# Kernel tuning notes

Hardware: AMD Instinct MI355X
Metric: run time of the kernel (lower is better)

The kernel has to match this reference:

```python
import jax, jax.numpy as jnp
import numpy as np
from jax import lax

B, N, C, RED = 8, 2048, 1024, 4
GN_EPS = 1e-5


def setup_inputs() -> dict:
    key = jax.random.key(0)
    ks = jax.random.split(key, 8)
    s = lambda k, shp, sc: jax.random.normal(k, shp, jnp.float32) * sc
    return dict(
        x=jax.random.normal(ks[0], (B, N, C), jnp.float32),
        qkv_w=s(ks[1], (C, 3 * C), 0.02),
        c1=jnp.float32(0.01 ** 2),
        c2=jnp.float32(0.03 ** 2),
        conv1_w=s(ks[2], (4, 1, 3), 0.3),      # OIH
        gn_g=jnp.ones(4, jnp.float32),
        gn_b=jnp.zeros(4, jnp.float32),
        conv2_w=s(ks[3], (1, 4, 3), 0.3),      # OIH
        conv2_b=jnp.zeros(1, jnp.float32),
        ch_w1=s(ks[4], (C, C // RED), 0.02),
        ch_b1=jnp.zeros(C // RED, jnp.float32),
        ch_w2=s(ks[5], (C // RED, C), 0.02),
        ch_b2=jnp.zeros(C, jnp.float32),
        proj_w=s(ks[6], (C, C), 0.02),
        proj_b=jnp.zeros(C, jnp.float32),
    )


def _conv1d(x, w):  # x:[B,Cin,N], w:[O,I,3], pad=1
    return lax.conv_general_dilated(x, w, (1,), [(1, 1)],
                                    dimension_numbers=('NCH', 'OIH', 'NCH'))


def _ode_func(A, conv1_w, gn_g, gn_b, conv2_w, conv2_b):
    # A: [B,N] -> Conv1d(1,4) -> GroupNorm(2,4) -> ReLU -> Conv1d(4,1)
    h = _conv1d(A[:, None, :], conv1_w)                 # [B,4,N]
    b, _, n = h.shape
    hg = h.reshape(b, 2, 2, n)                          # 2 groups of 2 channels
    mu = hg.mean((2, 3), keepdims=True)
    var = hg.var((2, 3), keepdims=True)
    h = ((hg - mu) * lax.rsqrt(var + GN_EPS)).reshape(b, 4, n)
    h = jax.nn.relu(h * gn_g[None, :, None] + gn_b[None, :, None])
    y = _conv1d(h, conv2_w) + conv2_b[None, :, None]    # [B,1,N]
    return y[:, 0, :]


def reference(x, qkv_w, c1, c2, conv1_w, gn_g, gn_b, conv2_w, conv2_b,
              ch_w1, ch_b1, ch_w2, ch_b2, proj_w, proj_b):
    Bx, Nx, Cx = x.shape
    qkv = (x @ qkv_w).reshape(Bx, Nx, 3, Cx)
    q, k, v = qkv[..., 0, :], qkv[..., 1, :], qkv[..., 2, :]

    # SSIM-style per-token statistics over the channel dim
    mu_q = q.mean(-1, keepdims=True)
    mu_k = k.mean(-1, keepdims=True)
    dq, dk = q - mu_q, k - mu_k
    inv_cm1 = 1.0 / (Cx - 1)
    sigma_qk = (dq * dk).sum(-1, keepdims=True) * inv_cm1
    sigma_q2 = (dq * dq).sum(-1, keepdims=True) * inv_cm1
    sigma_k2 = (dk * dk).sum(-1, keepdims=True) * inv_cm1
    num = (2 * mu_q * mu_k + c1) * (2 * sigma_qk + c2)
    den = (mu_q ** 2 + mu_k ** 2 + c1) * (sigma_q2 + sigma_k2 + c2)
    attn_base = ((num / (den + 1e-7)) ** 2)[..., 0]     # [B,N]

    # explicit-Euler integration over t = linspace(0,1,2) -> one step, dt=1
    steps = 2
    ts = jnp.linspace(0.0, 1.0, steps)
    dts = ts[1:] - ts[:-1]

    def step(A, dt):
        return A + dt * _ode_func(A, conv1_w, gn_g, gn_b, conv2_w, conv2_b), None

    A, _ = lax.scan(step, attn_base, dts)
    final_a = jax.nn.sigmoid(A)                         # [B,N]
    weights = jax.nn.softmax(final_a, axis=1)           # softmax over tokens

    # channel gating from mean token
    m = x.mean(axis=1, keepdims=True)                   # [B,1,C]
    ch_w = jax.nn.sigmoid(jax.nn.relu(m @ ch_w1 + ch_b1) @ ch_w2 + ch_b2)

    out_low = weights[..., None] * v * ch_w             # [B,N,C]
    return out_low @ proj_w + proj_b
```

## Files before the change

kernel.cpp:

```cpp
#include <hip/hip_runtime.h>

typedef __attribute__((ext_vector_type(8))) short short8;
typedef __attribute__((ext_vector_type(4))) short short4v;
typedef __attribute__((ext_vector_type(4))) float floatx4;

__device__ __forceinline__ unsigned short f2bf(float f) {
    unsigned u = __float_as_uint(f);
    u = u + 0x7fffu + ((u >> 16) & 1u);
    return (unsigned short)(u >> 16);
}
__device__ __forceinline__ float bf2f(short s) {
    return __uint_as_float(((unsigned)(unsigned short)s) << 16);
}

__device__ __forceinline__ void gl_lds16(const void* g, void* l) {
    __builtin_amdgcn_global_load_lds((const __attribute__((address_space(1))) void*)g,
                                     (__attribute__((address_space(3))) void*)l, 16, 0, 0);
}

__global__ __launch_bounds__(256) void convmean_kernel(const float* __restrict__ x,
                                                       short* __restrict__ xb,
                                                       float* __restrict__ part) {
    int bid = blockIdx.x;
    int b = bid >> 6, nch = bid & 63;
    int tid = threadIdx.x;
    size_t base = ((size_t)b * 2048 + nch * 32) * 1024;
    float s0 = 0.f, s1 = 0.f, s2 = 0.f, s3 = 0.f;
    int c0 = tid * 4;
    for (int r = 0; r < 32; r++) {
        const float* rp = x + base + (size_t)r * 1024 + c0;
        float4 v = *(const float4*)rp;
        s0 += v.x; s1 += v.y; s2 += v.z; s3 += v.w;
        short4v o;
        o[0] = (short)f2bf(v.x); o[1] = (short)f2bf(v.y);
        o[2] = (short)f2bf(v.z); o[3] = (short)f2bf(v.w);
        *(short4v*)(xb + base + (size_t)r * 1024 + c0) = o;
    }
    float* pp = part + ((size_t)b * 64 + nch) * 1024 + c0;
    float4 ps; ps.x = s0; ps.y = s1; ps.z = s2; ps.w = s3;
    *(float4*)pp = ps;
}

__global__ __launch_bounds__(256) void transpose_conv_kernel(const float* __restrict__ w_qkv,
                                                             short* __restrict__ qkvT,
                                                             const float* __restrict__ w_proj,
                                                             short* __restrict__ projT) {
    __shared__ float t[64][65];
    int bx = blockIdx.x;
    const float* in; short* out; int C;
    int c0, r0 = blockIdx.y * 64;
    if (bx < 48) { in = w_qkv; out = qkvT; C = 3072; c0 = bx * 64; }
    else         { in = w_proj; out = projT; C = 1024; c0 = (bx - 48) * 64; }
    int tid = threadIdx.x;
#pragma unroll
    for (int l = 0; l < 16; l++) {
        int idx = l * 256 + tid;
        int rr = idx >> 6, cc = idx & 63;
        t[rr][cc] = in[(size_t)(r0 + rr) * C + c0 + cc];
    }
    __syncthreads();
#pragma unroll
    for (int l = 0; l < 16; l++) {
        int idx = l * 256 + tid;
        int rr = idx >> 6, cc = idx & 63;
        out[(size_t)(c0 + rr) * 1024 + r0 + cc] = (short)f2bf(t[cc][rr]);
    }
}

__global__ __launch_bounds__(256) void ch_kernel(const float* __restrict__ part,
                                                 const float* __restrict__ w1,
                                                 const float* __restrict__ b1,
                                                 const float* __restrict__ w2,
                                                 const float* __restrict__ b2,
                                                 float* __restrict__ ch) {
    int b = blockIdx.x, tid = threadIdx.x;
    __shared__ float mrow[1024];
    __shared__ float hid[256];
    for (int i = tid; i < 1024; i += 256) {
        float s = 0.f;
        for (int j = 0; j < 64; j++) s += part[((size_t)b * 64 + j) * 1024 + i];
        mrow[i] = s * (1.f / 2048.f);
    }
    __syncthreads();
    {
        float s = 0.f;
        for (int i = 0; i < 1024; i++) s += mrow[i] * w1[(size_t)i * 256 + tid];
        hid[tid] = fmaxf(s + b1[tid], 0.f);
    }
    __syncthreads();
    for (int c = tid; c < 1024; c += 256) {
        float s = 0.f;
        for (int j = 0; j < 256; j++) s += hid[j] * w2[(size_t)j * 1024 + c];
        ch[(size_t)b * 1024 + c] = 1.f / (1.f + expf(-(s + b2[c])));
    }
}

__global__ __launch_bounds__(256) void gemm_qkv_kernel(const short* __restrict__ A,
                                                       const short* __restrict__ BT,
                                                       short* __restrict__ Cout,
                                                       const float* __restrict__ ch)
{
    __shared__ __align__(16) short Ash[2 * 128 * 32];
    __shared__ __align__(16) short Bsh[2 * 128 * 32];
    const int tid = threadIdx.x;
    const int wave = tid >> 6, lane = tid & 63;
    const int id = blockIdx.x;
    const int xcd = id & 7, j = id >> 3;
    const int bm = (j & 15) * 8 + xcd;
    const int bn = j >> 4;
    const int wm = wave >> 1, wn = wave & 1;
    const int l4 = lane >> 2, kk = (lane & 3) * 8;
    const int lda = 1024, ldb = 1024;

    const short* Ag = A + (size_t)(bm * 128 + wave * 32 + l4) * lda + kk;
    const short* Bg = BT + (size_t)(bn * 128 + wave * 32 + l4) * ldb + kk;
    short* lA = Ash + wave * 1024;
    short* lB = Bsh + wave * 1024;

    floatx4 acc[4][4];
    floatx4 zero = {0.f, 0.f, 0.f, 0.f};
#pragma unroll
    for (int i = 0; i < 4; i++)
#pragma unroll
        for (int jj = 0; jj < 4; jj++) acc[i][jj] = zero;

    const int ar = lane & 15, ak = (lane >> 4) * 8;

    for (int k0 = 0; k0 < 1024; k0 += 64) {
#pragma unroll
        for (int h = 0; h < 2; h++) {
            gl_lds16(Ag + k0 + h * 32, lA + h * 4096);
            gl_lds16(Ag + 16 * lda + k0 + h * 32, lA + h * 4096 + 512);
            gl_lds16(Bg + k0 + h * 32, lB + h * 4096);
            gl_lds16(Bg + 16 * ldb + k0 + h * 32, lB + h * 4096 + 512);
        }
        __syncthreads();
#pragma unroll
        for (int h = 0; h < 2; h++) {
            short8 af[4], bfr[4];
#pragma unroll
            for (int t = 0; t < 4; t++)
                af[t] = *(const short8*)(Ash + h * 4096 + (wm * 64 + t * 16 + ar) * 32 + ak);
#pragma unroll
            for (int t = 0; t < 4; t++)
                bfr[t] = *(const short8*)(Bsh + h * 4096 + (wn * 64 + t * 16 + ar) * 32 + ak);
#pragma unroll
            for (int i = 0; i < 4; i++)
#pragma unroll
                for (int jj = 0; jj < 4; jj++)
                    acc[i][jj] = __builtin_amdgcn_mfma_f32_16x16x32_bf16(af[i], bfr[jj], acc[i][jj], 0, 0, 0);
        }
        __syncthreads();
    }

    const int row0 = bm * 128 + wm * 64;
    const int col0 = bn * 128 + wn * 64;
#pragma unroll
    for (int i = 0; i < 4; i++) {
#pragma unroll
        for (int jj = 0; jj < 4; jj++) {
            int col = col0 + jj * 16 + (lane & 15);
#pragma unroll
            for (int r = 0; r < 4; r++) {
                int row = row0 + i * 16 + (lane >> 4) * 4 + r;
                float v = acc[i][jj][r];
                if (col >= 2048) v *= ch[(size_t)((row >> 11) << 10) + (col - 2048)];
                Cout[(size_t)row * 3072 + col] = (short)f2bf(v);
            }
        }
    }
}

__global__ __launch_bounds__(256) void stats_kernel(const short* __restrict__ qkv,
                                                    const float* __restrict__ c1p,
                                                    const float* __restrict__ c2p,
                                                    float* __restrict__ attn) {
    int row = blockIdx.x * 4 + (threadIdx.x >> 6);
    int lane = threadIdx.x & 63;
    const short* q = qkv + (size_t)row * 3072;
    const short* k = q + 1024;
    float sq = 0.f, sk = 0.f, sqq = 0.f, skk = 0.f, sqk = 0.f;
#pragma unroll
    for (int j = 0; j < 2; j++) {
        int idx = j * 512 + lane * 8;
        short8 qv = *(const short8*)(q + idx);
        short8 kv = *(const short8*)(k + idx);
#pragma unroll
        for (int e = 0; e < 8; e++) {
            float qf = bf2f(qv[e]), kf = bf2f(kv[e]);
            sq += qf; sk += kf;
            sqq += qf * qf; skk += kf * kf; sqk += qf * kf;
        }
    }
#pragma unroll
    for (int m = 1; m < 64; m <<= 1) {
        sq += __shfl_xor(sq, m);
        sk += __shfl_xor(sk, m);
        sqq += __shfl_xor(sqq, m);
        skk += __shfl_xor(skk, m);
        sqk += __shfl_xor(sqk, m);
    }
    if (lane == 0) {
        const float C = 1024.f, invcm1 = 1.f / 1023.f;
        float c1 = *c1p, c2 = *c2p;
        float muq = sq / C, muk = sk / C;
        float sigqk = (sqk - C * muq * muk) * invcm1;
        float sigq2 = (sqq - C * muq * muq) * invcm1;
        float sigk2 = (skk - C * muk * muk) * invcm1;
        float num = (2.f * muq * muk + c1) * (2.f * sigqk + c2);
        float den = (muq * muq + muk * muk + c1) * (sigq2 + sigk2 + c2);
        float r = num / (den + 1e-7f);
        attn[row] = r * r;
    }
}

__device__ __forceinline__ float blk_sum(float v, float* buf) {
#pragma unroll
    for (int m = 1; m < 64; m <<= 1) v += __shfl_xor(v, m);
    int wave = threadIdx.x >> 6;
    if ((threadIdx.x & 63) == 0) buf[wave] = v;
    __syncthreads();
    float r = buf[0] + buf[1] + buf[2] + buf[3];
    __syncthreads();
    return r;
}
__device__ __forceinline__ float blk_max(float v, float* buf) {
#pragma unroll
    for (int m = 1; m < 64; m <<= 1) v = fmaxf(v, __shfl_xor(v, m));
    int wave = threadIdx.x >> 6;
    if ((threadIdx.x & 63) == 0) buf[wave] = v;
    __syncthreads();
    float r = fmaxf(fmaxf(buf[0], buf[1]), fmaxf(buf[2], buf[3]));
    __syncthreads();
    return r;
}

__global__ __launch_bounds__(256) void ode_softmax_kernel(const float* __restrict__ attn,
                                                          const float* __restrict__ w1,
                                                          const float* __restrict__ gng,
                                                          const float* __restrict__ gnb,
                                                          const float* __restrict__ w2,
                                                          const float* __restrict__ b2,
                                                          float* __restrict__ wgt) {
    int b = blockIdx.x, tid = threadIdx.x;
    __shared__ float A0[2048];
    __shared__ float H[4][2048];
    __shared__ float rbuf[4];
    for (int i = tid; i < 2048; i += 256) A0[i] = attn[(size_t)b * 2048 + i];
    __syncthreads();
    float w1l[12], w2l[12];
#pragma unroll
    for (int i = 0; i < 12; i++) { w1l[i] = w1[i]; w2l[i] = w2[i]; }
    float gg[4], gb[4];
#pragma unroll
    for (int c = 0; c < 4; c++) { gg[c] = gng[c]; gb[c] = gnb[c]; }

    float s0 = 0.f, ss0 = 0.f, s1 = 0.f, ss1 = 0.f;
    for (int i = tid; i < 2048; i += 256) {
        float le = (i > 0) ? A0[i - 1] : 0.f;
        float mi = A0[i];
        float ri = (i < 2047) ? A0[i + 1] : 0.f;
#pragma unroll
        for (int c = 0; c < 4; c++) {
            float h = w1l[c * 3] * le + w1l[c * 3 + 1] * mi + w1l[c * 3 + 2] * ri;
            H[c][i] = h;
            if (c < 2) { s0 += h; ss0 += h * h; } else { s1 += h; ss1 += h * h; }
        }
    }
    s0 = blk_sum(s0, rbuf);
    ss0 = blk_sum(ss0, rbuf);
    s1 = blk_sum(s1, rbuf);
    ss1 = blk_sum(ss1, rbuf);
    float mu0 = s0 / 4096.f, var0 = ss0 / 4096.f - mu0 * mu0;
    float mu1 = s1 / 4096.f, var1 = ss1 / 4096.f - mu1 * mu1;
    float is0 = 1.f / sqrtf(var0 + 1e-5f);
    float is1 = 1.f / sqrtf(var1 + 1e-5f);

    for (int i = tid; i < 2048; i += 256) {
#pragma unroll
        for (int c = 0; c < 4; c++) {
            float inv = (c < 2) ? is0 : is1;
            float mu = (c < 2) ? mu0 : mu1;
            float v = (H[c][i] - mu) * inv * gg[c] + gb[c];
            H[c][i] = fmaxf(v, 0.f);
        }
    }
    __syncthreads();

    float bias2 = b2[0];
    float myfa[8];
    float lmax = -1e30f;
#pragma unroll
    for (int ii = 0; ii < 8; ii++) {
        int i = tid + ii * 256;
        float y = bias2;
#pragma unroll
        for (int c = 0; c < 4; c++) {
            float le = (i > 0) ? H[c][i - 1] : 0.f;
            float mi = H[c][i];
            float ri = (i < 2047) ? H[c][i + 1] : 0.f;
            y += w2l[c * 3] * le + w2l[c * 3 + 1] * mi + w2l[c * 3 + 2] * ri;
        }
        float Av = A0[i] + y;
        float fa = 1.f / (1.f + expf(-Av));
        myfa[ii] = fa;
        lmax = fmaxf(lmax, fa);
    }
    float gmax = blk_max(lmax, rbuf);
    float lsum = 0.f;
#pragma unroll
    for (int ii = 0; ii < 8; ii++) {
        myfa[ii] = expf(myfa[ii] - gmax);
        lsum += myfa[ii];
    }
    float gsum = blk_sum(lsum, rbuf);
    float inv = 1.f / gsum;
#pragma unroll
    for (int ii = 0; ii < 8; ii++) wgt[(size_t)b * 2048 + tid + ii * 256] = myfa[ii] * inv;
}

__global__ __launch_bounds__(256) void gemm_out_kernel(const short* __restrict__ qkv,
                                                       const short* __restrict__ BT,
                                                       const float* __restrict__ wgt,
                                                       const float* __restrict__ pb,
                                                       float* __restrict__ Out)
{
    __shared__ __align__(16) short Ash[2 * 128 * 32];
    __shared__ __align__(16) short Bsh[2 * 128 * 32];
    const int tid = threadIdx.x;
    const int wave = tid >> 6, lane = tid & 63;
    const int id = blockIdx.x;
    const int xcd = id & 7, j = id >> 3;
    const int bm = (j & 15) * 8 + xcd;
    const int bn = j >> 4;
    const int wm = wave >> 1, wn = wave & 1;
    const int l4 = lane >> 2, kk = (lane & 3) * 8;
    const int lda = 3072, ldb = 1024;
    const short* A = qkv + 2048;

    const short* Ag = A + (size_t)(bm * 128 + wave * 32 + l4) * lda + kk;
    const short* Bg = BT + (size_t)(bn * 128 + wave * 32 + l4) * ldb + kk;
    short* lA = Ash + wave * 1024;
    short* lB = Bsh + wave * 1024;

    floatx4 acc[4][4];
    floatx4 zero = {0.f, 0.f, 0.f, 0.f};
#pragma unroll
    for (int i = 0; i < 4; i++)
#pragma unroll
        for (int jj = 0; jj < 4; jj++) acc[i][jj] = zero;

    const int ar = lane & 15, ak = (lane >> 4) * 8;

    for (int k0 = 0; k0 < 1024; k0 += 64) {
#pragma unroll
        for (int h = 0; h < 2; h++) {
            gl_lds16(Ag + k0 + h * 32, lA + h * 4096);
            gl_lds16(Ag + 16 * lda + k0 + h * 32, lA + h * 4096 + 512);
            gl_lds16(Bg + k0 + h * 32, lB + h * 4096);
            gl_lds16(Bg + 16 * ldb + k0 + h * 32, lB + h * 4096 + 512);
        }
        __syncthreads();
#pragma unroll
        for (int h = 0; h < 2; h++) {
            short8 af[4], bfr[4];
#pragma unroll
            for (int t = 0; t < 4; t++)
                af[t] = *(const short8*)(Ash + h * 4096 + (wm * 64 + t * 16 + ar) * 32 + ak);
#pragma unroll
            for (int t = 0; t < 4; t++)
                bfr[t] = *(const short8*)(Bsh + h * 4096 + (wn * 64 + t * 16 + ar) * 32 + ak);
#pragma unroll
            for (int i = 0; i < 4; i++)
#pragma unroll
                for (int jj = 0; jj < 4; jj++)
                    acc[i][jj] = __builtin_amdgcn_mfma_f32_16x16x32_bf16(af[i], bfr[jj], acc[i][jj], 0, 0, 0);
        }
        __syncthreads();
    }

    const int row0 = bm * 128 + wm * 64;
    const int col0 = bn * 128 + wn * 64;
#pragma unroll
    for (int i = 0; i < 4; i++) {
#pragma unroll
        for (int jj = 0; jj < 4; jj++) {
            int col = col0 + jj * 16 + (lane & 15);
            float bias = pb[col];
#pragma unroll
            for (int r = 0; r < 4; r++) {
                int row = row0 + i * 16 + (lane >> 4) * 4 + r;
                Out[(size_t)row * 1024 + col] = wgt[row] * acc[i][jj][r] + bias;
            }
        }
    }
}

extern "C" void kernel_launch(void* const* d_in, const int* in_sizes, int n_in,
                              void* d_out, int out_size, void* d_ws, size_t ws_size,
                              hipStream_t stream) {
    const float* x       = (const float*)d_in[0];
    const float* qkv_w   = (const float*)d_in[1];
    const float* c1      = (const float*)d_in[2];
    const float* c2      = (const float*)d_in[3];
    const float* conv1_w = (const float*)d_in[4];
    const float* gn_g    = (const float*)d_in[5];
    const float* gn_b    = (const float*)d_in[6];
    const float* conv2_w = (const float*)d_in[7];
    const float* conv2_b = (const float*)d_in[8];
    const float* ch_w1   = (const float*)d_in[9];
    const float* ch_b1   = (const float*)d_in[10];
    const float* ch_w2   = (const float*)d_in[11];
    const float* ch_b2   = (const float*)d_in[12];
    const float* proj_w  = (const float*)d_in[13];
    const float* proj_b  = (const float*)d_in[14];
    float* out = (float*)d_out;

    size_t off = 0;
    char* base = (char*)d_ws;
    auto carve = [&](size_t bytes) -> char* {
        char* p = base + off;
        off += (bytes + 255) & ~(size_t)255;
        return p;
    };
    short* x_bf  = (short*)carve((size_t)16777216 * 2);
    short* qkvT  = (short*)carve((size_t)3072 * 1024 * 2);
    short* projT = (short*)carve((size_t)1024 * 1024 * 2);
    short* qkv   = (short*)carve((size_t)16384 * 3072 * 2);
    float* attn  = (float*)carve((size_t)16384 * 4);
    float* wgt   = (float*)carve((size_t)16384 * 4);
    float* part  = (float*)carve((size_t)8 * 64 * 1024 * 4);
    float* chw   = (float*)carve((size_t)8 * 1024 * 4);

    convmean_kernel<<<512, 256, 0, stream>>>(x, x_bf, part);
    transpose_conv_kernel<<<dim3(64, 16), 256, 0, stream>>>(qkv_w, qkvT, proj_w, projT);
    ch_kernel<<<8, 256, 0, stream>>>(part, ch_w1, ch_b1, ch_w2, ch_b2, chw);
    gemm_qkv_kernel<<<3072, 256, 0, stream>>>(x_bf, qkvT, qkv, chw);
    stats_kernel<<<4096, 256, 0, stream>>>(qkv, c1, c2, attn);
    ode_softmax_kernel<<<8, 256, 0, stream>>>(attn, conv1_w, gn_g, gn_b, conv2_w, conv2_b, wgt);
    gemm_out_kernel<<<1024, 256, 0, stream>>>(qkv, projT, wgt, proj_b, out);
}
```

Baseline: 456.2 us.

## Fuse SSIM q/k statistics into QKV GEMM epilogue and skip writing q,k

Interleaves q and k weight rows so each GEMM tile holds paired q/k columns, and computes per-row partial sums (sum q, sum k, q², k², qk) in the epilogue instead of storing q and k. A small finalize kernel reduces the 16 partials into the SSIM attention value, which removes the stats kernel and the q/k write and read traffic. V is written to a compact buffer through LDS-staged, vectorized stores. The output GEMM also stages its results in LDS for coalesced float4 stores. Block-to-tile mapping is reordered in both GEMMs. Computing statistics from fp32 accumulators rather than bf16-rounded values slightly changes numerics.

```diff
diff --git a/kernel.cpp b/kernel.cpp
--- a/kernel.cpp
+++ b/kernel.cpp
@@ -47,10 +47,10 @@
                                                              short* __restrict__ projT) {
     __shared__ float t[64][65];
     int bx = blockIdx.x;
-    const float* in; short* out; int C;
+    const float* in; short* out; int C; bool is_qkv;
     int c0, r0 = blockIdx.y * 64;
-    if (bx < 48) { in = w_qkv; out = qkvT; C = 3072; c0 = bx * 64; }
-    else         { in = w_proj; out = projT; C = 1024; c0 = (bx - 48) * 64; }
+    if (bx < 48) { in = w_qkv; out = qkvT; C = 3072; c0 = bx * 64; is_qkv = true; }
+    else         { in = w_proj; out = projT; C = 1024; c0 = (bx - 48) * 64; is_qkv = false; }
     int tid = threadIdx.x;
 #pragma unroll
     for (int l = 0; l < 16; l++) {
@@ -63,7 +63,13 @@
     for (int l = 0; l < 16; l++) {
         int idx = l * 256 + tid;
         int rr = idx >> 6, cc = idx & 63;
-        out[(size_t)(c0 + rr) * 1024 + r0 + cc] = (short)f2bf(t[cc][rr]);
+        int ro = c0 + rr;
+        int rnew = ro;
+        if (is_qkv) {
+            if (ro < 1024) rnew = 2 * ro;
+            else if (ro < 2048) rnew = 2 * (ro - 1024) + 1;
+        }
+        out[(size_t)rnew * 1024 + r0 + cc] = (short)f2bf(t[cc][rr]);
     }
 }
 
@@ -97,8 +103,9 @@
 
 __global__ __launch_bounds__(256) void gemm_qkv_kernel(const short* __restrict__ A,
                                                        const short* __restrict__ BT,
-                                                       short* __restrict__ Cout,
-                                                       const float* __restrict__ ch)
+                                                       short* __restrict__ vbuf,
+                                                       const float* __restrict__ ch,
+                                                       float* __restrict__ part2)
 {
     __shared__ __align__(16) short Ash[2 * 128 * 32];
     __shared__ __align__(16) short Bsh[2 * 128 * 32];
@@ -106,8 +113,11 @@
     const int wave = tid >> 6, lane = tid & 63;
     const int id = blockIdx.x;
     const int xcd = id & 7, j = id >> 3;
-    const int bm = (j & 15) * 8 + xcd;
-    const int bn = j >> 4;
+    const int half = j / 192;
+    const int rem = j % 192;
+    const int bmi = rem & 7;
+    const int bn = rem >> 3;
+    const int bm = (half * 8 + bmi) * 8 + xcd;
     const int wm = wave >> 1, wn = wave & 1;
     const int l4 = lane >> 2, kk = (lane & 3) * 8;
     const int lda = 1024, ldb = 1024;
@@ -125,6 +135,7 @@
         for (int jj = 0; jj < 4; jj++) acc[i][jj] = zero;
 
     const int ar = lane & 15, ak = (lane >> 4) * 8;
+    const int quad = lane >> 4;
 
     for (int k0 = 0; k0 < 1024; k0 += 64) {
 #pragma unroll
@@ -153,65 +164,101 @@
         __syncthreads();
     }
 
-    const int row0 = bm * 128 + wm * 64;
-    const int col0 = bn * 128 + wn * 64;
-#pragma unroll
-    for (int i = 0; i < 4; i++) {
-#pragma unroll
-        for (int jj = 0; jj < 4; jj++) {
-            int col = col0 + jj * 16 + (lane & 15);
-#pragma unroll
-            for (int r = 0; r < 4; r++) {
-                int row = row0 + i * 16 + (lane >> 4) * 4 + r;
-                float v = acc[i][jj][r];
-                if (col >= 2048) v *= ch[(size_t)((row >> 11) << 10) + (col - 2048)];
-                Cout[(size_t)row * 3072 + col] = (short)f2bf(v);
+    if (bn < 16) {
+        float* sb = (float*)Ash;
+#pragma unroll
+        for (int i = 0; i < 4; i++) {
+            float st[4][5];
+#pragma unroll
+            for (int r = 0; r < 4; r++)
+#pragma unroll
+                for (int f = 0; f < 5; f++) st[r][f] = 0.f;
+#pragma unroll
+            for (int jj = 0; jj < 4; jj++) {
+#pragma unroll
+                for (int r = 0; r < 4; r++) {
+                    float val = acc[i][jj][r];
+                    float other = __shfl_xor(val, 1);
+                    float q = (lane & 1) ? other : val;
+                    float kv = (lane & 1) ? val : other;
+                    st[r][0] += q; st[r][1] += kv;
+                    st[r][2] += q * q; st[r][3] += kv * kv; st[r][4] += q * kv;
+                }
             }
-        }
-    }
-}
-
-__global__ __launch_bounds__(256) void stats_kernel(const short* __restrict__ qkv,
-                                                    const float* __restrict__ c1p,
-                                                    const float* __restrict__ c2p,
-                                                    float* __restrict__ attn) {
-    int row = blockIdx.x * 4 + (threadIdx.x >> 6);
-    int lane = threadIdx.x & 63;
-    const short* q = qkv + (size_t)row * 3072;
-    const short* k = q + 1024;
-    float sq = 0.f, sk = 0.f, sqq = 0.f, skk = 0.f, sqk = 0.f;
-#pragma unroll
-    for (int j = 0; j < 2; j++) {
-        int idx = j * 512 + lane * 8;
-        short8 qv = *(const short8*)(q + idx);
-        short8 kv = *(const short8*)(k + idx);
-#pragma unroll
-        for (int e = 0; e < 8; e++) {
-            float qf = bf2f(qv[e]), kf = bf2f(kv[e]);
-            sq += qf; sk += kf;
-            sqq += qf * qf; skk += kf * kf; sqk += qf * kf;
-        }
-    }
-#pragma unroll
-    for (int m = 1; m < 64; m <<= 1) {
-        sq += __shfl_xor(sq, m);
-        sk += __shfl_xor(sk, m);
-        sqq += __shfl_xor(sqq, m);
-        skk += __shfl_xor(skk, m);
-        sqk += __shfl_xor(sqk, m);
-    }
-    if (lane == 0) {
-        const float C = 1024.f, invcm1 = 1.f / 1023.f;
-        float c1 = *c1p, c2 = *c2p;
-        float muq = sq / C, muk = sk / C;
-        float sigqk = (sqk - C * muq * muk) * invcm1;
-        float sigq2 = (sqq - C * muq * muq) * invcm1;
-        float sigk2 = (skk - C * muk * muk) * invcm1;
-        float num = (2.f * muq * muk + c1) * (2.f * sigqk + c2);
-        float den = (muq * muq + muk * muk + c1) * (sigq2 + sigk2 + c2);
-        float r = num / (den + 1e-7f);
-        attn[row] = r * r;
-    }
+#pragma unroll
+            for (int r = 0; r < 4; r++)
+#pragma unroll
+                for (int f = 0; f < 5; f++) {
+                    float v = st[r][f];
+                    v += __shfl_xor(v, 2);
+                    v += __shfl_xor(v, 4);
+                    v += __shfl_xor(v, 8);
+                    st[r][f] = v;
+                }
+            if ((lane & 15) == 0) {
+#pragma unroll
+                for (int r = 0; r < 4; r++)
+#pragma unroll
+                    for (int f = 0; f < 5; f++)
+                        sb[(size_t)(wn * 128 + wm * 64 + i * 16 + quad * 4 + r) * 5 + f] = st[r][f];
+            }
+        }
+        __syncthreads();
+        if (tid < 128) {
+            int grow = bm * 128 + tid;
+#pragma unroll
+            for (int f = 0; f < 5; f++) {
+                float s = sb[(size_t)tid * 5 + f] + sb[(size_t)(128 + tid) * 5 + f];
+                part2[(size_t)(bn * 5 + f) * 16384 + grow] = s;
+            }
+        }
+    } else {
+        const int batch = (bm * 128) >> 11;
+        const int vcol0 = bn * 128 - 2048 + wn * 64;
+        short* pbuf = Ash + wave * 1024;
+        float cw[4];
+#pragma unroll
+        for (int jj = 0; jj < 4; jj++) cw[jj] = ch[(size_t)batch * 1024 + vcol0 + jj * 16 + ar];
+#pragma unroll
+        for (int i = 0; i < 4; i++) {
+#pragma unroll
+            for (int jj = 0; jj < 4; jj++)
+#pragma unroll
+                for (int r = 0; r < 4; r++)
+                    pbuf[(quad * 4 + r) * 64 + jj * 16 + ar] = (short)f2bf(acc[i][jj][r] * cw[jj]);
+#pragma unroll
+            for (int p = 0; p < 2; p++) {
+                int idx = p * 512 + lane * 8;
+                short8 vv = *(const short8*)(pbuf + idx);
+                int grow = bm * 128 + wm * 64 + i * 16 + (idx >> 6);
+                int gcol = vcol0 + (idx & 63);
+                *(short8*)(vbuf + (size_t)grow * 1024 + gcol) = vv;
+            }
+        }
+    }
+}
+
+__global__ __launch_bounds__(256) void finalize_kernel(const float* __restrict__ part2,
+                                                       const float* __restrict__ c1p,
+                                                       const float* __restrict__ c2p,
+                                                       float* __restrict__ attn) {
+    int row = blockIdx.x * 256 + threadIdx.x;
+    float s[5] = {0.f, 0.f, 0.f, 0.f, 0.f};
+#pragma unroll
+    for (int slot = 0; slot < 16; slot++)
+#pragma unroll
+        for (int f = 0; f < 5; f++)
+            s[f] += part2[(size_t)((slot * 5 + f) << 14) + row];
+    const float C = 1024.f, invcm1 = 1.f / 1023.f;
+    float c1 = *c1p, c2 = *c2p;
+    float muq = s[0] / C, muk = s[1] / C;
+    float sigqk = (s[4] - C * muq * muk) * invcm1;
+    float sigq2 = (s[2] - C * muq * muq) * invcm1;
+    float sigk2 = (s[3] - C * muk * muk) * invcm1;
+    float num = (2.f * muq * muk + c1) * (2.f * sigqk + c2);
+    float den = (muq * muq + muk * muk + c1) * (sigq2 + sigk2 + c2);
+    float r = num / (den + 1e-7f);
+    attn[row] = r * r;
 }
 
 __device__ __forceinline__ float blk_sum(float v, float* buf) {
@@ -319,7 +366,7 @@
     for (int ii = 0; ii < 8; ii++) wgt[(size_t)b * 2048 + tid + ii * 256] = myfa[ii] * inv;
 }
 
-__global__ __launch_bounds__(256) void gemm_out_kernel(const short* __restrict__ qkv,
+__global__ __launch_bounds__(256) void gemm_out_kernel(const short* __restrict__ vbuf,
                                                        const short* __restrict__ BT,
                                                        const float* __restrict__ wgt,
                                                        const float* __restrict__ pb,
@@ -331,14 +378,16 @@
     const int wave = tid >> 6, lane = tid & 63;
     const int id = blockIdx.x;
     const int xcd = id & 7, j = id >> 3;
-    const int bm = (j & 15) * 8 + xcd;
-    const int bn = j >> 4;
+    const int half = j >> 6;
+    const int rem = j & 63;
+    const int bmi = rem & 7;
+    const int bn = rem >> 3;
+    const int bm = (half * 8 + bmi) * 8 + xcd;
     const int wm = wave >> 1, wn = wave & 1;
     const int l4 = lane >> 2, kk = (lane & 3) * 8;
-    const int lda = 3072, ldb = 1024;
-    const short* A = qkv + 2048;
-
-    const short* Ag = A + (size_t)(bm * 128 + wave * 32 + l4) * lda + kk;
+    const int lda = 1024, ldb = 1024;
+
+    const short* Ag = vbuf + (size_t)(bm * 128 + wave * 32 + l4) * lda + kk;
     const short* Bg = BT + (size_t)(bn * 128 + wave * 32 + l4) * ldb + kk;
     short* lA = Ash + wave * 1024;
     short* lB = Bsh + wave * 1024;
@@ -351,6 +400,7 @@
         for (int jj = 0; jj < 4; jj++) acc[i][jj] = zero;
 
     const int ar = lane & 15, ak = (lane >> 4) * 8;
+    const int quad = lane >> 4;
 
     for (int k0 = 0; k0 < 1024; k0 += 64) {
 #pragma unroll
@@ -381,17 +431,25 @@
 
     const int row0 = bm * 128 + wm * 64;
     const int col0 = bn * 128 + wn * 64;
+    float* obuf = (float*)Ash + wave * 1024;
 #pragma unroll
     for (int i = 0; i < 4; i++) {
 #pragma unroll
         for (int jj = 0; jj < 4; jj++) {
-            int col = col0 + jj * 16 + (lane & 15);
-            float bias = pb[col];
+            float bias = pb[col0 + jj * 16 + ar];
 #pragma unroll
             for (int r = 0; r < 4; r++) {
-                int row = row0 + i * 16 + (lane >> 4) * 4 + r;
-                Out[(size_t)row * 1024 + col] = wgt[row] * acc[i][jj][r] + bias;
+                int grow = row0 + i * 16 + quad * 4 + r;
+                obuf[(quad * 4 + r) * 64 + jj * 16 + ar] = wgt[grow] * acc[i][jj][r] + bias;
             }
+        }
+#pragma unroll
+        for (int p = 0; p < 4; p++) {
+            int idx = p * 256 + lane * 4;
+            float4 vv = *(const float4*)(obuf + idx);
+            int grow = row0 + i * 16 + (idx >> 6);
+            int gcol = col0 + (idx & 63);
+            *(float4*)(Out + (size_t)grow * 1024 + gcol) = vv;
         }
     }
 }
@@ -423,10 +481,11 @@
         off += (bytes + 255) & ~(size_t)255;
         return p;
     };
-    short* x_bf  = (short*)carve((size_t)16777216 * 2);
+    short* x_bf  = (short*)carve((size_t)16384 * 1024 * 2);
     short* qkvT  = (short*)carve((size_t)3072 * 1024 * 2);
     short* projT = (short*)carve((size_t)1024 * 1024 * 2);
-    short* qkv   = (short*)carve((size_t)16384 * 3072 * 2);
+    short* vbuf  = (short*)carve((size_t)16384 * 1024 * 2);
+    float* part2 = (float*)carve((size_t)80 * 16384 * 4);
     float* attn  = (float*)carve((size_t)16384 * 4);
     float* wgt   = (float*)carve((size_t)16384 * 4);
     float* part  = (float*)carve((size_t)8 * 64 * 1024 * 4);
@@ -435,8 +494,8 @@
     convmean_kernel<<<512, 256, 0, stream>>>(x, x_bf, part);
     transpose_conv_kernel<<<dim3(64, 16), 256, 0, stream>>>(qkv_w, qkvT, proj_w, projT);
     ch_kernel<<<8, 256, 0, stream>>>(part, ch_w1, ch_b1, ch_w2, ch_b2, chw);
-    gemm_qkv_kernel<<<3072, 256, 0, stream>>>(x_bf, qkvT, qkv, chw);
-    stats_kernel<<<4096, 256, 0, stream>>>(qkv, c1, c2, attn);
+    gemm_qkv_kernel<<<3072, 256, 0, stream>>>(x_bf, qkvT, vbuf, chw, part2);
+    finalize_kernel<<<64, 256, 0, stream>>>(part2, c1, c2, attn);
     ode_softmax_kernel<<<8, 256, 0, stream>>>(attn, conv1_w, gn_g, gn_b, conv2_w, conv2_b, wgt);
-    gemm_out_kernel<<<1024, 256, 0, stream>>>(qkv, projT, wgt, proj_b, out);
-}
+    gemm_out_kernel<<<1024, 256, 0, stream>>>(vbuf, projT, wgt, proj_b, out);
+}
```

Result: slower. 539.3 us (+18.2%).
